# Performance work log

Measured on AMD Instinct MI355X. Metric: run time of the kernel, lower is better.

Reference implementation:

```python
import jax, jax.numpy as jnp
import numpy as np
import math

DIM = 2048
N_HEADS = 32
N_KV_HEADS = 8
HEAD_DIM = DIM // N_HEADS  # 64
N_REP = N_HEADS // N_KV_HEADS  # 4
BSZ, SEQ = 2, 2048


def setup_inputs() -> dict:
    key = jax.random.key(0)
    ks = jax.random.split(key, 8)
    x = jax.random.normal(ks[0], (BSZ, SEQ, DIM), dtype=jnp.float32)
    # rotary tables, [seq, head_dim//2]
    inv_freq = 1.0 / (10000.0 ** (np.arange(0, HEAD_DIM, 2, dtype=np.float32) / HEAD_DIM))
    t = np.arange(SEQ, dtype=np.float32)
    freqs = np.outer(t, inv_freq)
    freqs_cos = jnp.asarray(np.cos(freqs))
    freqs_sin = jnp.asarray(np.sin(freqs))
    s = 0.02
    wq = jax.random.normal(ks[1], (DIM, N_HEADS * HEAD_DIM), dtype=jnp.float32) * s
    wk = jax.random.normal(ks[2], (DIM, N_KV_HEADS * HEAD_DIM), dtype=jnp.float32) * s
    wv = jax.random.normal(ks[3], (DIM, N_KV_HEADS * HEAD_DIM), dtype=jnp.float32) * s
    wo = jax.random.normal(ks[4], (N_HEADS * HEAD_DIM, DIM), dtype=jnp.float32) * s
    return {"x": x, "freqs_cos": freqs_cos, "freqs_sin": freqs_sin,
            "wq": wq, "wk": wk, "wv": wv, "wo": wo}


def _apply_rotary(xq, xk, cos, sin):
    # xq: [b,s,h,d], xk: [b,s,kh,d]; cos/sin: [s, d//2]
    def rot(t):
        tr = t[..., 0::2]  # even -> real
        ti = t[..., 1::2]  # odd  -> imag
        c = cos[None, :, None, :]
        s_ = sin[None, :, None, :]
        or_ = tr * c - ti * s_
        oi_ = tr * s_ + ti * c
        # interleave back: [..., d//2, 2] -> [..., d]
        return jnp.stack([or_, oi_], axis=-1).reshape(t.shape)
    return rot(xq), rot(xk)


def reference(x, freqs_cos, freqs_sin, wq, wk, wv, wo):
    b, s, _ = x.shape
    xq = (x @ wq).reshape(b, s, N_HEADS, HEAD_DIM)
    xk = (x @ wk).reshape(b, s, N_KV_HEADS, HEAD_DIM)
    xv = (x @ wv).reshape(b, s, N_KV_HEADS, HEAD_DIM)
    xq, xk = _apply_rotary(xq, xk, freqs_cos, freqs_sin)
    # repeat_kv: [b,s,kh,d] -> [b,s,kh*n_rep,d]
    xk = jnp.repeat(xk, N_REP, axis=2)
    xv = jnp.repeat(xv, N_REP, axis=2)
    # [b,h,s,d]
    q = xq.transpose(0, 2, 1, 3)
    k = xk.transpose(0, 2, 1, 3)
    v = xv.transpose(0, 2, 1, 3)
    scale = 1.0 / math.sqrt(HEAD_DIM)
    scores = jnp.einsum('bhqd,bhkd->bhqk', q, k) * scale
    causal = jnp.tril(jnp.ones((s, s), dtype=bool))
    scores = jnp.where(causal[None, None], scores, jnp.float32(-jnp.inf))
    probs = jax.nn.softmax(scores, axis=-1)
    out = jnp.einsum('bhqk,bhkd->bhqd', probs, v)  # [b,h,s,d]
    out = out.transpose(0, 2, 1, 3).reshape(b, s, N_HEADS * HEAD_DIM)
    return out @ wo
```

## Files before the change

kernel.cpp:

```cpp
#include <hip/hip_runtime.h>
#include <hip/hip_bf16.h>

typedef __attribute__((ext_vector_type(8))) short short8;
typedef __attribute__((ext_vector_type(4))) float f32x4;

__device__ __forceinline__ unsigned short f2bf(float f) {
  union { float f; unsigned u; } v; v.f = f;
  unsigned r = v.u + 0x7FFFu + ((v.u >> 16) & 1u);
  return (unsigned short)(r >> 16);
}
__device__ __forceinline__ float bf2f(unsigned short h) {
  union { unsigned u; float f; } v; v.u = ((unsigned)h) << 16;
  return v.f;
}
__device__ __forceinline__ unsigned pkbf(float a, float b) {
  __hip_bfloat162 h = __float22bfloat162_rn(float2{a, b});
  union { __hip_bfloat162 h; unsigned u; } cv; cv.h = h;
  return cv.u;
}

__global__ void prep(const float* __restrict__ x, const float* __restrict__ wq,
                     const float* __restrict__ wk, const float* __restrict__ wv,
                     const float* __restrict__ wo, unsigned short* __restrict__ xb,
                     unsigned short* __restrict__ wt, unsigned short* __restrict__ wot) {
  const int z = blockIdx.z, tid = threadIdx.x;
  if (z == 0) {
    int id = blockIdx.y * 64 + blockIdx.x;
#pragma unroll
    for (int rep = 0; rep < 2; ++rep) {
      int i = (rep * 4096 + id) * 256 + tid;
      float4 v = ((const float4*)x)[i];
      ushort4 o;
      o.x = f2bf(v.x); o.y = f2bf(v.y); o.z = f2bf(v.z); o.w = f2bf(v.w);
      ((ushort4*)xb)[i] = o;
    }
    return;
  }
  __shared__ float tile[32][33];
  const float* src;
  unsigned short* dst;
  int N;
  if (z == 1) { src = wq; dst = wt; N = 2048; }
  else if (z == 2) { src = wk; dst = wt + 2048ull * 2048; N = 512; }
  else if (z == 3) { src = wv; dst = wt + 2560ull * 2048; N = 512; }
  else { src = wo; dst = wot; N = 2048; }
  const int K = 2048;
  int n0 = blockIdx.x * 32, k0 = blockIdx.y * 32;
  if (n0 >= N) return;
  int xx = tid & 31, yy = tid >> 5;
#pragma unroll
  for (int j = 0; j < 4; ++j) tile[yy + 8 * j][xx] = src[(size_t)(k0 + yy + 8 * j) * N + n0 + xx];
  __syncthreads();
#pragma unroll
  for (int j = 0; j < 4; ++j) dst[(size_t)(n0 + yy + 8 * j) * K + k0 + xx] = f2bf(tile[xx][yy + 8 * j]);
}

template <int MODE>
__global__ __launch_bounds__(256, 2) void gemm_bt64(const unsigned short* __restrict__ A,
                                                    const unsigned short* __restrict__ Bt,
                                                    void* __restrict__ Cv, int K, int ldc,
                                                    unsigned short* __restrict__ vt) {
  __shared__ alignas(16) unsigned short As[128 * 64];
  __shared__ alignas(16) unsigned short Bs[128 * 64];
  const int t = threadIdx.x;
  const int lane = t & 63, w = t >> 6;
  const int l15 = lane & 15, quad = lane >> 4;
  const int bn0 = blockIdx.x * 128, bm0 = blockIdx.y * 128;
  const int wm = (w >> 1) * 64, wn = (w & 1) * 64;
  const unsigned short* Ab = A + (size_t)bm0 * K;
  const unsigned short* Bb = Bt + (size_t)bn0 * K;
  const int asw = l15 & 7;

  f32x4 acc[4][4];
  const f32x4 zf = {0.f, 0.f, 0.f, 0.f};
#pragma unroll
  for (int i = 0; i < 4; ++i)
#pragma unroll
    for (int j = 0; j < 4; ++j) acc[i][j] = zf;

  for (int k0 = 0; k0 < K; k0 += 64) {
    __syncthreads();
#pragma unroll
    for (int r = 0; r < 4; ++r) {
      int e = r * 256 + t;
      int row = e >> 3, cslot = e & 7;
      int cg = cslot ^ (row & 7);
      const unsigned short* ga = Ab + (size_t)row * K + k0 + cg * 8;
      __builtin_amdgcn_global_load_lds((const __attribute__((address_space(1))) void*)ga,
                                       (__attribute__((address_space(3))) void*)(As + e * 8), 16, 0, 0);
      const unsigned short* gb = Bb + (size_t)row * K + k0 + cg * 8;
      __builtin_amdgcn_global_load_lds((const __attribute__((address_space(1))) void*)gb,
                                       (__attribute__((address_space(3))) void*)(Bs + e * 8), 16, 0, 0);
    }
    __syncthreads();
#pragma unroll
    for (int s = 0; s < 2; ++s) {
      short8 af[4], bf[4];
#pragma unroll
      for (int i = 0; i < 4; ++i)
        af[i] = *reinterpret_cast<const short8*>(As + (wm + i * 16 + l15) * 64 + (((s * 4 + quad) ^ asw) * 8));
#pragma unroll
      for (int j = 0; j < 4; ++j)
        bf[j] = *reinterpret_cast<const short8*>(Bs + (wn + j * 16 + l15) * 64 + (((s * 4 + quad) ^ asw) * 8));
#pragma unroll
      for (int i = 0; i < 4; ++i)
#pragma unroll
        for (int j = 0; j < 4; ++j)
          acc[i][j] = __builtin_amdgcn_mfma_f32_16x16x32_bf16(af[i], bf[j], acc[i][j], 0, 0, 0);
    }
  }

  if (MODE == 1 && bn0 >= 2560) {
    const int b = bm0 >> 11;
#pragma unroll
    for (int i = 0; i < 4; ++i) {
      int srow = (bm0 + wm + i * 16 + quad * 4) & 2047;
#pragma unroll
      for (int j = 0; j < 4; ++j) {
        int vcol = bn0 - 2560 + wn + j * 16 + l15;
        int kvh = vcol >> 6, d = vcol & 63;
        uint2 pk = make_uint2(pkbf(acc[i][j][0], acc[i][j][1]), pkbf(acc[i][j][2], acc[i][j][3]));
        *reinterpret_cast<uint2*>(vt + ((size_t)(b * 8 + kvh) * 64 + d) * 2048 + srow) = pk;
      }
    }
  } else {
#pragma unroll
    for (int i = 0; i < 4; ++i)
#pragma unroll
      for (int j = 0; j < 4; ++j)
#pragma unroll
        for (int r = 0; r < 4; ++r) {
          size_t row = (size_t)(bm0 + wm + i * 16 + quad * 4 + r);
          size_t col = (size_t)(bn0 + wn + j * 16 + l15);
          if (MODE == 1)
            ((unsigned short*)Cv)[row * ldc + col] = f2bf(acc[i][j][r]);
          else
            ((float*)Cv)[row * ldc + col] = acc[i][j][r];
        }
  }
}

__global__ void rope_k(unsigned short* __restrict__ qkv, const float* __restrict__ fcos,
                       const float* __restrict__ fsin) {
  int tid = blockIdx.x * 256 + threadIdx.x;
  int row = tid >> 8, p = tid & 255;
  int col = 2048 + 2 * p;
  int s = row & 2047;
  int fi = p & 31;
  float c = fcos[s * 32 + fi], sn = fsin[s * 32 + fi];
  unsigned int* ptr = (unsigned int*)(qkv + (size_t)row * 2560 + col);
  unsigned int pr = *ptr;
  float xr = bf2f((unsigned short)(pr & 0xFFFFu));
  float xi = bf2f((unsigned short)(pr >> 16));
  float orr = xr * c - xi * sn;
  float oi = xr * sn + xi * c;
  *ptr = ((unsigned)f2bf(oi) << 16) | (unsigned)f2bf(orr);
}

__global__ __launch_bounds__(256, 4) void flash_attn(const unsigned short* __restrict__ qkv,
                                                     const unsigned short* __restrict__ vt,
                                                     const float* __restrict__ fcos,
                                                     const float* __restrict__ fsin,
                                                     unsigned short* __restrict__ out) {
  __shared__ alignas(16) unsigned short Ks[64 * 64];
  __shared__ alignas(16) unsigned short Vs[64 * 64];
  __shared__ alignas(16) unsigned short Ps[128 * 64];
  __shared__ float Ls[128];
  const int t = threadIdx.x, lane = t & 63, w = t >> 6;
  const int l15 = lane & 15, quad = lane >> 4;
  const int h = blockIdx.y, b = blockIdx.z;
  const int qb = ((int)blockIdx.x ^ (15 * (h >> 4))) & 15;
  const int q0 = qb * 128;
  const int kvh = h >> 2;
  const size_t rowB = (size_t)b * 2048;
  const unsigned short* Qg = qkv + (rowB + q0) * 2560 + h * 64;
  const unsigned short* Kg = qkv + rowB * 2560 + 2048 + kvh * 64;
  const unsigned short* Vtg = vt + (size_t)(b * 8 + kvh) * 64 * 2048;
  const float SC = 0.18033688011112042f;

  short8 qf[2][2];
#pragma unroll
  for (int mt = 0; mt < 2; ++mt)
#pragma unroll
    for (int s = 0; s < 2; ++s) {
      int qrow = w * 32 + mt * 16 + l15;
      short8 raw = *reinterpret_cast<const short8*>(Qg + (size_t)qrow * 2560 + s * 32 + quad * 8);
      f32x4 c4 = *reinterpret_cast<const f32x4*>(fcos + (size_t)(q0 + qrow) * 32 + s * 16 + quad * 4);
      f32x4 s4 = *reinterpret_cast<const f32x4*>(fsin + (size_t)(q0 + qrow) * 32 + s * 16 + quad * 4);
      short8 o;
#pragma unroll
      for (int k = 0; k < 4; ++k) {
        float xr = bf2f((unsigned short)raw[2 * k]);
        float xi = bf2f((unsigned short)raw[2 * k + 1]);
        o[2 * k] = (short)f2bf((xr * c4[k] - xi * s4[k]) * SC);
        o[2 * k + 1] = (short)f2bf((xr * s4[k] + xi * c4[k]) * SC);
      }
      qf[mt][s] = o;
    }

  const f32x4 zf = {0.f, 0.f, 0.f, 0.f};
  f32x4 oacc[2][4];
#pragma unroll
  for (int mt = 0; mt < 2; ++mt)
#pragma unroll
    for (int nt = 0; nt < 4; ++nt) oacc[mt][nt] = zf;
  float lsum[2] = {0.f, 0.f};

  const int kb_end = 2 * qb + 2;
  const int srow = t >> 3, sc8 = t & 7;
  const int soff = srow * 64 + ((sc8 ^ (srow & 7)) * 8);
  const int asw = l15 & 7;
  short8 kreg[2], vreg[2];
#pragma unroll
  for (int r = 0; r < 2; ++r) {
    kreg[r] = *reinterpret_cast<const short8*>(Kg + (size_t)(srow + 32 * r) * 2560 + sc8 * 8);
    vreg[r] = *reinterpret_cast<const short8*>(Vtg + (size_t)(srow + 32 * r) * 2048 + sc8 * 8);
  }

  for (int kb = 0; kb < kb_end; ++kb) {
    __syncthreads();
#pragma unroll
    for (int r = 0; r < 2; ++r) {
      *reinterpret_cast<short8*>(Ks + soff + r * 32 * 64) = kreg[r];
      *reinterpret_cast<short8*>(Vs + soff + r * 32 * 64) = vreg[r];
    }
    __syncthreads();
    if (kb + 1 < kb_end) {
#pragma unroll
      for (int r = 0; r < 2; ++r) {
        kreg[r] = *reinterpret_cast<const short8*>(Kg + (size_t)((kb + 1) * 64 + srow + 32 * r) * 2560 + sc8 * 8);
        vreg[r] = *reinterpret_cast<const short8*>(Vtg + (size_t)(srow + 32 * r) * 2048 + (kb + 1) * 64 + sc8 * 8);
      }
    }
    const int qmaxw = q0 + w * 32 + 31;
    if (kb * 64 > qmaxw) continue;
    const bool needMask = (kb * 64 + 63) > (q0 + w * 32);

#pragma unroll
    for (int kvt = 0; kvt < 4; ++kvt) {
      f32x4 st0 = zf, st1 = zf;
#pragma unroll
      for (int s = 0; s < 2; ++s) {
        short8 kf = *reinterpret_cast<const short8*>(Ks + (kvt * 16 + l15) * 64 + ((s * 4 + quad) ^ asw) * 8);
        st0 = __builtin_amdgcn_mfma_f32_16x16x32_bf16(kf, qf[0][s], st0, 0, 0, 0);
        st1 = __builtin_amdgcn_mfma_f32_16x16x32_bf16(kf, qf[1][s], st1, 0, 0, 0);
      }
      const int pcol = ((kvt * 2 + (quad >> 1)) ^ asw) * 8 + (quad & 1) * 4;
      if (needMask) {
        const int kvb = kb * 64 + kvt * 16 + quad * 4;
#pragma unroll
        for (int qt = 0; qt < 2; ++qt) {
          const f32x4 stv = qt ? st1 : st0;
          const int qg = q0 + w * 32 + qt * 16 + l15;
          float p[4];
#pragma unroll
          for (int r = 0; r < 4; ++r) {
            float pv = __builtin_amdgcn_exp2f(stv[r]);
            p[r] = (kvb + r > qg) ? 0.f : pv;
          }
          lsum[qt] += (p[0] + p[1]) + (p[2] + p[3]);
          *reinterpret_cast<uint2*>(Ps + (size_t)(w * 32 + qt * 16 + l15) * 64 + pcol) =
              make_uint2(pkbf(p[0], p[1]), pkbf(p[2], p[3]));
        }
      } else {
#pragma unroll
        for (int qt = 0; qt < 2; ++qt) {
          const f32x4 stv = qt ? st1 : st0;
          float p[4];
#pragma unroll
          for (int r = 0; r < 4; ++r) p[r] = __builtin_amdgcn_exp2f(stv[r]);
          lsum[qt] += (p[0] + p[1]) + (p[2] + p[3]);
          *reinterpret_cast<uint2*>(Ps + (size_t)(w * 32 + qt * 16 + l15) * 64 + pcol) =
              make_uint2(pkbf(p[0], p[1]), pkbf(p[2], p[3]));
        }
      }
    }

#pragma unroll
    for (int s = 0; s < 2; ++s) {
      short8 vf[4];
#pragma unroll
      for (int nt = 0; nt < 4; ++nt)
        vf[nt] = *reinterpret_cast<const short8*>(Vs + (nt * 16 + l15) * 64 + ((s * 4 + quad) ^ asw) * 8);
#pragma unroll
      for (int mt = 0; mt < 2; ++mt) {
        short8 pf = *reinterpret_cast<const short8*>(Ps + (size_t)(w * 32 + mt * 16 + l15) * 64 + ((s * 4 + quad) ^ asw) * 8);
#pragma unroll
        for (int nt = 0; nt < 4; ++nt)
          oacc[mt][nt] = __builtin_amdgcn_mfma_f32_16x16x32_bf16(pf, vf[nt], oacc[mt][nt], 0, 0, 0);
      }
    }
  }

#pragma unroll
  for (int qt = 0; qt < 2; ++qt) {
    lsum[qt] += __shfl_xor(lsum[qt], 16, 64);
    lsum[qt] += __shfl_xor(lsum[qt], 32, 64);
  }
  if (quad == 0) {
    Ls[w * 32 + l15] = lsum[0];
    Ls[w * 32 + 16 + l15] = lsum[1];
  }
  float linv[2][4];
#pragma unroll
  for (int mt = 0; mt < 2; ++mt)
#pragma unroll
    for (int r = 0; r < 4; ++r) linv[mt][r] = 1.f / Ls[w * 32 + mt * 16 + quad * 4 + r];

#pragma unroll
  for (int mt = 0; mt < 2; ++mt)
#pragma unroll
    for (int nt = 0; nt < 4; ++nt)
#pragma unroll
      for (int r = 0; r < 4; ++r) {
        size_t row = rowB + (size_t)(q0 + w * 32 + mt * 16 + quad * 4 + r);
        size_t col = (size_t)h * 64 + nt * 16 + l15;
        out[row * 2048 + col] = f2bf(oacc[mt][nt][r] * linv[mt][r]);
      }
}

extern "C" void kernel_launch(void* const* d_in, const int* in_sizes, int n_in, void* d_out,
                              int out_size, void* d_ws, size_t ws_size, hipStream_t stream) {
  const float* x = (const float*)d_in[0];
  const float* fcos = (const float*)d_in[1];
  const float* fsin = (const float*)d_in[2];
  const float* wq = (const float*)d_in[3];
  const float* wk = (const float*)d_in[4];
  const float* wv = (const float*)d_in[5];
  const float* wo = (const float*)d_in[6];

  char* ws = (char*)d_ws;
  unsigned short* xb = (unsigned short*)ws;
  unsigned short* wt = (unsigned short*)(ws + 16777216ull);
  unsigned short* wot = (unsigned short*)(ws + 29360128ull);
  unsigned short* qkv = (unsigned short*)(ws + 37748736ull);
  unsigned short* attno = (unsigned short*)(ws + 58720256ull);
  unsigned short* vt = (unsigned short*)(ws + 75497472ull);

  prep<<<dim3(64, 64, 5), 256, 0, stream>>>(x, wq, wk, wv, wo, xb, wt, wot);
  gemm_bt64<1><<<dim3(24, 32), 256, 0, stream>>>(xb, wt, qkv, 2048, 2560, vt);
  rope_k<<<4096, 256, 0, stream>>>(qkv, fcos, fsin);
  flash_attn<<<dim3(16, 32, 2), 256, 0, stream>>>(qkv, vt, fcos, fsin, attno);
  gemm_bt64<0><<<dim3(16, 32), 256, 0, stream>>>(attno, wot, d_out, 2048, 2048, nullptr);
}
```

Measured before the change: 271.0 us.

## Fuse K rope into QKV GEMM epilogue and pair causal query tiles in attention

The K-part rotary embedding moves into the QKV GEMM epilogue, using a lane shuffle to fetch the pair element, and the separate rope kernel is dropped. Flash attention now processes two query tiles per block (qb and 15-qb) so every block does the same causal work. K/V tiles are double-buffered in LDS via global_load_lds async copies, and row sums are computed with an MFMA against a ones vector. The cost is higher register and LDS use, which is why launch bounds drop to 2 blocks per SM, and the grid is halved.

```diff
diff --git a/kernel.cpp b/kernel.cpp
--- a/kernel.cpp
+++ b/kernel.cpp
@@ -59,7 +59,9 @@
 __global__ __launch_bounds__(256, 2) void gemm_bt64(const unsigned short* __restrict__ A,
                                                     const unsigned short* __restrict__ Bt,
                                                     void* __restrict__ Cv, int K, int ldc,
-                                                    unsigned short* __restrict__ vt) {
+                                                    unsigned short* __restrict__ vt,
+                                                    const float* __restrict__ fcos,
+                                                    const float* __restrict__ fsin) {
   __shared__ alignas(16) unsigned short As[128 * 64];
   __shared__ alignas(16) unsigned short Bs[128 * 64];
   const int t = threadIdx.x;
@@ -123,6 +125,23 @@
         *reinterpret_cast<uint2*>(vt + ((size_t)(b * 8 + kvh) * 64 + d) * 2048 + srow) = pk;
       }
     }
+  } else if (MODE == 1 && bn0 >= 2048) {
+#pragma unroll
+    for (int i = 0; i < 4; ++i)
+#pragma unroll
+      for (int j = 0; j < 4; ++j)
+#pragma unroll
+        for (int r = 0; r < 4; ++r) {
+          int row = bm0 + wm + i * 16 + quad * 4 + r;
+          int s = row & 2047;
+          int col = bn0 + wn + j * 16 + l15;
+          int fi = ((col - 2048) >> 1) & 31;
+          float val = acc[i][j][r];
+          float par = __shfl_xor(val, 1, 64);
+          float c = fcos[s * 32 + fi], sn = fsin[s * 32 + fi];
+          float o = (lane & 1) ? (par * sn + val * c) : (val * c - par * sn);
+          ((unsigned short*)Cv)[(size_t)row * ldc + col] = f2bf(o);
+        }
   } else {
 #pragma unroll
     for (int i = 0; i < 4; ++i)
@@ -140,137 +159,153 @@
   }
 }
 
-__global__ void rope_k(unsigned short* __restrict__ qkv, const float* __restrict__ fcos,
-                       const float* __restrict__ fsin) {
-  int tid = blockIdx.x * 256 + threadIdx.x;
-  int row = tid >> 8, p = tid & 255;
-  int col = 2048 + 2 * p;
-  int s = row & 2047;
-  int fi = p & 31;
-  float c = fcos[s * 32 + fi], sn = fsin[s * 32 + fi];
-  unsigned int* ptr = (unsigned int*)(qkv + (size_t)row * 2560 + col);
-  unsigned int pr = *ptr;
-  float xr = bf2f((unsigned short)(pr & 0xFFFFu));
-  float xi = bf2f((unsigned short)(pr >> 16));
-  float orr = xr * c - xi * sn;
-  float oi = xr * sn + xi * c;
-  *ptr = ((unsigned)f2bf(oi) << 16) | (unsigned)f2bf(orr);
-}
-
-__global__ __launch_bounds__(256, 4) void flash_attn(const unsigned short* __restrict__ qkv,
+__global__ __launch_bounds__(256, 2) void flash_attn(const unsigned short* __restrict__ qkv,
                                                      const unsigned short* __restrict__ vt,
                                                      const float* __restrict__ fcos,
                                                      const float* __restrict__ fsin,
                                                      unsigned short* __restrict__ out) {
-  __shared__ alignas(16) unsigned short Ks[64 * 64];
-  __shared__ alignas(16) unsigned short Vs[64 * 64];
-  __shared__ alignas(16) unsigned short Ps[128 * 64];
-  __shared__ float Ls[128];
+  __shared__ alignas(16) unsigned short Ks[2][64 * 64];
+  __shared__ alignas(16) unsigned short Vs[2][64 * 64];
+  __shared__ alignas(16) unsigned short Ps[256 * 64];
   const int t = threadIdx.x, lane = t & 63, w = t >> 6;
   const int l15 = lane & 15, quad = lane >> 4;
   const int h = blockIdx.y, b = blockIdx.z;
-  const int qb = ((int)blockIdx.x ^ (15 * (h >> 4))) & 15;
-  const int q0 = qb * 128;
+  const int qb = blockIdx.x;
+  const int qA0 = qb * 128, qB0 = (15 - qb) * 128;
   const int kvh = h >> 2;
   const size_t rowB = (size_t)b * 2048;
-  const unsigned short* Qg = qkv + (rowB + q0) * 2560 + h * 64;
   const unsigned short* Kg = qkv + rowB * 2560 + 2048 + kvh * 64;
   const unsigned short* Vtg = vt + (size_t)(b * 8 + kvh) * 64 * 2048;
   const float SC = 0.18033688011112042f;
 
-  short8 qf[2][2];
-#pragma unroll
-  for (int mt = 0; mt < 2; ++mt)
-#pragma unroll
-    for (int s = 0; s < 2; ++s) {
-      int qrow = w * 32 + mt * 16 + l15;
-      short8 raw = *reinterpret_cast<const short8*>(Qg + (size_t)qrow * 2560 + s * 32 + quad * 8);
-      f32x4 c4 = *reinterpret_cast<const f32x4*>(fcos + (size_t)(q0 + qrow) * 32 + s * 16 + quad * 4);
-      f32x4 s4 = *reinterpret_cast<const f32x4*>(fsin + (size_t)(q0 + qrow) * 32 + s * 16 + quad * 4);
-      short8 o;
-#pragma unroll
-      for (int k = 0; k < 4; ++k) {
-        float xr = bf2f((unsigned short)raw[2 * k]);
-        float xi = bf2f((unsigned short)raw[2 * k + 1]);
-        o[2 * k] = (short)f2bf((xr * c4[k] - xi * s4[k]) * SC);
-        o[2 * k + 1] = (short)f2bf((xr * s4[k] + xi * c4[k]) * SC);
-      }
-      qf[mt][s] = o;
-    }
+  short8 qfA[2][2], qfB[2][2];
+#pragma unroll
+  for (int tl = 0; tl < 2; ++tl) {
+    const int q0 = tl ? qB0 : qA0;
+    const unsigned short* Qg = qkv + (rowB + q0) * 2560 + h * 64;
+#pragma unroll
+    for (int mt = 0; mt < 2; ++mt)
+#pragma unroll
+      for (int s = 0; s < 2; ++s) {
+        int qrow = w * 32 + mt * 16 + l15;
+        short8 raw = *reinterpret_cast<const short8*>(Qg + (size_t)qrow * 2560 + s * 32 + quad * 8);
+        f32x4 c4 = *reinterpret_cast<const f32x4*>(fcos + (size_t)(q0 + qrow) * 32 + s * 16 + quad * 4);
+        f32x4 s4 = *reinterpret_cast<const f32x4*>(fsin + (size_t)(q0 + qrow) * 32 + s * 16 + quad * 4);
+        short8 o;
+#pragma unroll
+        for (int k = 0; k < 4; ++k) {
+          float xr = bf2f((unsigned short)raw[2 * k]);
+          float xi = bf2f((unsigned short)raw[2 * k + 1]);
+          o[2 * k] = (short)f2bf((xr * c4[k] - xi * s4[k]) * SC);
+          o[2 * k + 1] = (short)f2bf((xr * s4[k] + xi * c4[k]) * SC);
+        }
+        if (tl) qfB[mt][s] = o; else qfA[mt][s] = o;
+      }
+  }
 
   const f32x4 zf = {0.f, 0.f, 0.f, 0.f};
-  f32x4 oacc[2][4];
-#pragma unroll
-  for (int mt = 0; mt < 2; ++mt)
-#pragma unroll
-    for (int nt = 0; nt < 4; ++nt) oacc[mt][nt] = zf;
-  float lsum[2] = {0.f, 0.f};
-
-  const int kb_end = 2 * qb + 2;
-  const int srow = t >> 3, sc8 = t & 7;
-  const int soff = srow * 64 + ((sc8 ^ (srow & 7)) * 8);
+  f32x4 oaccA[2][4], oaccB[2][4], laccA[2], laccB[2];
+#pragma unroll
+  for (int mt = 0; mt < 2; ++mt) {
+    laccA[mt] = zf; laccB[mt] = zf;
+#pragma unroll
+    for (int nt = 0; nt < 4; ++nt) { oaccA[mt][nt] = zf; oaccB[mt][nt] = zf; }
+  }
+  short8 onesf;
+#pragma unroll
+  for (int k = 0; k < 8; ++k) onesf[k] = (short)0x3F80;
+
+  const int kbB_end = 32 - 2 * qb;
   const int asw = l15 & 7;
-  short8 kreg[2], vreg[2];
-#pragma unroll
-  for (int r = 0; r < 2; ++r) {
-    kreg[r] = *reinterpret_cast<const short8*>(Kg + (size_t)(srow + 32 * r) * 2560 + sc8 * 8);
-    vreg[r] = *reinterpret_cast<const short8*>(Vtg + (size_t)(srow + 32 * r) * 2048 + sc8 * 8);
-  }
-
-  for (int kb = 0; kb < kb_end; ++kb) {
+  unsigned short* Ks0 = &Ks[0][0];
+  unsigned short* Ks1 = &Ks[1][0];
+  unsigned short* Vs0 = &Vs[0][0];
+  unsigned short* Vs1 = &Vs[1][0];
+
+  auto stage = [&](int buf, int kb) {
+    unsigned short* kd = buf ? Ks1 : Ks0;
+    unsigned short* vd = buf ? Vs1 : Vs0;
+#pragma unroll
+    for (int r = 0; r < 2; ++r) {
+      int e = r * 256 + t;
+      int row = e >> 3, cs = e & 7;
+      int cg = cs ^ (row & 7);
+      const unsigned short* gk = Kg + (size_t)(kb * 64 + row) * 2560 + cg * 8;
+      __builtin_amdgcn_global_load_lds((const __attribute__((address_space(1))) void*)gk,
+                                       (__attribute__((address_space(3))) void*)(kd + e * 8), 16, 0, 0);
+      const unsigned short* gv = Vtg + (size_t)row * 2048 + kb * 64 + cg * 8;
+      __builtin_amdgcn_global_load_lds((const __attribute__((address_space(1))) void*)gv,
+                                       (__attribute__((address_space(3))) void*)(vd + e * 8), 16, 0, 0);
+    }
+  };
+
+  stage(0, 0);
+
+  for (int kb = 0; kb < kbB_end; ++kb) {
+    const int cur = kb & 1;
     __syncthreads();
-#pragma unroll
-    for (int r = 0; r < 2; ++r) {
-      *reinterpret_cast<short8*>(Ks + soff + r * 32 * 64) = kreg[r];
-      *reinterpret_cast<short8*>(Vs + soff + r * 32 * 64) = vreg[r];
-    }
-    __syncthreads();
-    if (kb + 1 < kb_end) {
-#pragma unroll
-      for (int r = 0; r < 2; ++r) {
-        kreg[r] = *reinterpret_cast<const short8*>(Kg + (size_t)((kb + 1) * 64 + srow + 32 * r) * 2560 + sc8 * 8);
-        vreg[r] = *reinterpret_cast<const short8*>(Vtg + (size_t)(srow + 32 * r) * 2048 + (kb + 1) * 64 + sc8 * 8);
-      }
-    }
-    const int qmaxw = q0 + w * 32 + 31;
-    if (kb * 64 > qmaxw) continue;
-    const bool needMask = (kb * 64 + 63) > (q0 + w * 32);
+    if (kb + 1 < kbB_end) stage(cur ^ 1, kb + 1);
+    const unsigned short* Kc = cur ? Ks1 : Ks0;
+    const unsigned short* Vc = cur ? Vs1 : Vs0;
+    const bool actA = kb * 64 <= qA0 + w * 32 + 31;
+    const bool actB = kb * 64 <= qB0 + w * 32 + 31;
+    const bool mA = (kb * 64 + 63) > (qA0 + w * 32);
+    const bool mB = (kb * 64 + 63) > (qB0 + w * 32);
 
 #pragma unroll
     for (int kvt = 0; kvt < 4; ++kvt) {
-      f32x4 st0 = zf, st1 = zf;
+      f32x4 sA0 = zf, sA1 = zf, sB0 = zf, sB1 = zf;
 #pragma unroll
       for (int s = 0; s < 2; ++s) {
-        short8 kf = *reinterpret_cast<const short8*>(Ks + (kvt * 16 + l15) * 64 + ((s * 4 + quad) ^ asw) * 8);
-        st0 = __builtin_amdgcn_mfma_f32_16x16x32_bf16(kf, qf[0][s], st0, 0, 0, 0);
-        st1 = __builtin_amdgcn_mfma_f32_16x16x32_bf16(kf, qf[1][s], st1, 0, 0, 0);
+        short8 kf = *reinterpret_cast<const short8*>(Kc + (kvt * 16 + l15) * 64 + ((s * 4 + quad) ^ asw) * 8);
+        if (actA) {
+          sA0 = __builtin_amdgcn_mfma_f32_16x16x32_bf16(kf, qfA[0][s], sA0, 0, 0, 0);
+          sA1 = __builtin_amdgcn_mfma_f32_16x16x32_bf16(kf, qfA[1][s], sA1, 0, 0, 0);
+        }
+        if (actB) {
+          sB0 = __builtin_amdgcn_mfma_f32_16x16x32_bf16(kf, qfB[0][s], sB0, 0, 0, 0);
+          sB1 = __builtin_amdgcn_mfma_f32_16x16x32_bf16(kf, qfB[1][s], sB1, 0, 0, 0);
+        }
       }
       const int pcol = ((kvt * 2 + (quad >> 1)) ^ asw) * 8 + (quad & 1) * 4;
-      if (needMask) {
-        const int kvb = kb * 64 + kvt * 16 + quad * 4;
+      const int kvb = kb * 64 + kvt * 16 + quad * 4;
+      if (actA) {
 #pragma unroll
         for (int qt = 0; qt < 2; ++qt) {
-          const f32x4 stv = qt ? st1 : st0;
-          const int qg = q0 + w * 32 + qt * 16 + l15;
+          const f32x4 stv = qt ? sA1 : sA0;
           float p[4];
-#pragma unroll
-          for (int r = 0; r < 4; ++r) {
-            float pv = __builtin_amdgcn_exp2f(stv[r]);
-            p[r] = (kvb + r > qg) ? 0.f : pv;
+          if (mA) {
+            const int qg = qA0 + w * 32 + qt * 16 + l15;
+#pragma unroll
+            for (int r = 0; r < 4; ++r) {
+              float pv = __builtin_amdgcn_exp2f(stv[r]);
+              p[r] = (kvb + r > qg) ? 0.f : pv;
+            }
+          } else {
+#pragma unroll
+            for (int r = 0; r < 4; ++r) p[r] = __builtin_amdgcn_exp2f(stv[r]);
           }
-          lsum[qt] += (p[0] + p[1]) + (p[2] + p[3]);
           *reinterpret_cast<uint2*>(Ps + (size_t)(w * 32 + qt * 16 + l15) * 64 + pcol) =
               make_uint2(pkbf(p[0], p[1]), pkbf(p[2], p[3]));
         }
-      } else {
+      }
+      if (actB) {
 #pragma unroll
         for (int qt = 0; qt < 2; ++qt) {
-          const f32x4 stv = qt ? st1 : st0;
+          const f32x4 stv = qt ? sB1 : sB0;
           float p[4];
-#pragma unroll
-          for (int r = 0; r < 4; ++r) p[r] = __builtin_amdgcn_exp2f(stv[r]);
-          lsum[qt] += (p[0] + p[1]) + (p[2] + p[3]);
-          *reinterpret_cast<uint2*>(Ps + (size_t)(w * 32 + qt * 16 + l15) * 64 + pcol) =
+          if (mB) {
+            const int qg = qB0 + w * 32 + qt * 16 + l15;
+#pragma unroll
+            for (int r = 0; r < 4; ++r) {
+              float pv = __builtin_amdgcn_exp2f(stv[r]);
+              p[r] = (kvb + r > qg) ? 0.f : pv;
+            }
+          } else {
+#pragma unroll
+            for (int r = 0; r < 4; ++r) p[r] = __builtin_amdgcn_exp2f(stv[r]);
+          }
+          *reinterpret_cast<uint2*>(Ps + (size_t)(128 + w * 32 + qt * 16 + l15) * 64 + pcol) =
               make_uint2(pkbf(p[0], p[1]), pkbf(p[2], p[3]));
         }
       }
@@ -281,42 +316,49 @@
       short8 vf[4];
 #pragma unroll
       for (int nt = 0; nt < 4; ++nt)
-        vf[nt] = *reinterpret_cast<const short8*>(Vs + (nt * 16 + l15) * 64 + ((s * 4 + quad) ^ asw) * 8);
-#pragma unroll
-      for (int mt = 0; mt < 2; ++mt) {
-        short8 pf = *reinterpret_cast<const short8*>(Ps + (size_t)(w * 32 + mt * 16 + l15) * 64 + ((s * 4 + quad) ^ asw) * 8);
-#pragma unroll
-        for (int nt = 0; nt < 4; ++nt)
-          oacc[mt][nt] = __builtin_amdgcn_mfma_f32_16x16x32_bf16(pf, vf[nt], oacc[mt][nt], 0, 0, 0);
-      }
-    }
-  }
-
-#pragma unroll
-  for (int qt = 0; qt < 2; ++qt) {
-    lsum[qt] += __shfl_xor(lsum[qt], 16, 64);
-    lsum[qt] += __shfl_xor(lsum[qt], 32, 64);
-  }
-  if (quad == 0) {
-    Ls[w * 32 + l15] = lsum[0];
-    Ls[w * 32 + 16 + l15] = lsum[1];
-  }
-  float linv[2][4];
-#pragma unroll
-  for (int mt = 0; mt < 2; ++mt)
-#pragma unroll
-    for (int r = 0; r < 4; ++r) linv[mt][r] = 1.f / Ls[w * 32 + mt * 16 + quad * 4 + r];
-
-#pragma unroll
-  for (int mt = 0; mt < 2; ++mt)
-#pragma unroll
-    for (int nt = 0; nt < 4; ++nt)
+        vf[nt] = *reinterpret_cast<const short8*>(Vc + (nt * 16 + l15) * 64 + ((s * 4 + quad) ^ asw) * 8);
+      if (actA) {
+#pragma unroll
+        for (int mt = 0; mt < 2; ++mt) {
+          short8 pf = *reinterpret_cast<const short8*>(Ps + (size_t)(w * 32 + mt * 16 + l15) * 64 + ((s * 4 + quad) ^ asw) * 8);
+#pragma unroll
+          for (int nt = 0; nt < 4; ++nt)
+            oaccA[mt][nt] = __builtin_amdgcn_mfma_f32_16x16x32_bf16(pf, vf[nt], oaccA[mt][nt], 0, 0, 0);
+          laccA[mt] = __builtin_amdgcn_mfma_f32_16x16x32_bf16(pf, onesf, laccA[mt], 0, 0, 0);
+        }
+      }
+      if (actB) {
+#pragma unroll
+        for (int mt = 0; mt < 2; ++mt) {
+          short8 pf = *reinterpret_cast<const short8*>(Ps + (size_t)(128 + w * 32 + mt * 16 + l15) * 64 + ((s * 4 + quad) ^ asw) * 8);
+#pragma unroll
+          for (int nt = 0; nt < 4; ++nt)
+            oaccB[mt][nt] = __builtin_amdgcn_mfma_f32_16x16x32_bf16(pf, vf[nt], oaccB[mt][nt], 0, 0, 0);
+          laccB[mt] = __builtin_amdgcn_mfma_f32_16x16x32_bf16(pf, onesf, laccB[mt], 0, 0, 0);
+        }
+      }
+    }
+  }
+
+#pragma unroll
+  for (int tl = 0; tl < 2; ++tl) {
+    const int q0 = tl ? qB0 : qA0;
+#pragma unroll
+    for (int mt = 0; mt < 2; ++mt) {
+      const f32x4 lv = tl ? laccB[mt] : laccA[mt];
 #pragma unroll
       for (int r = 0; r < 4; ++r) {
+        const float linv = 1.f / lv[r];
         size_t row = rowB + (size_t)(q0 + w * 32 + mt * 16 + quad * 4 + r);
-        size_t col = (size_t)h * 64 + nt * 16 + l15;
-        out[row * 2048 + col] = f2bf(oacc[mt][nt][r] * linv[mt][r]);
-      }
+#pragma unroll
+        for (int nt = 0; nt < 4; ++nt) {
+          const f32x4 ov = tl ? oaccB[mt][nt] : oaccA[mt][nt];
+          size_t col = (size_t)h * 64 + nt * 16 + l15;
+          out[row * 2048 + col] = f2bf(ov[r] * linv);
+        }
+      }
+    }
+  }
 }
 
 extern "C" void kernel_launch(void* const* d_in, const int* in_sizes, int n_in, void* d_out,
@@ -338,8 +380,7 @@
   unsigned short* vt = (unsigned short*)(ws + 75497472ull);
 
   prep<<<dim3(64, 64, 5), 256, 0, stream>>>(x, wq, wk, wv, wo, xb, wt, wot);
-  gemm_bt64<1><<<dim3(24, 32), 256, 0, stream>>>(xb, wt, qkv, 2048, 2560, vt);
-  rope_k<<<4096, 256, 0, stream>>>(qkv, fcos, fsin);
-  flash_attn<<<dim3(16, 32, 2), 256, 0, stream>>>(qkv, vt, fcos, fsin, attno);
-  gemm_bt64<0><<<dim3(16, 32), 256, 0, stream>>>(attno, wot, d_out, 2048, 2048, nullptr);
-}
+  gemm_bt64<1><<<dim3(24, 32), 256, 0, stream>>>(xb, wt, qkv, 2048, 2560, vt, fcos, fsin);
+  flash_attn<<<dim3(8, 32, 2), 256, 0, stream>>>(qkv, vt, fcos, fsin, attno);
+  gemm_bt64<0><<<dim3(16, 32), 256, 0, stream>>>(attno, wot, d_out, 2048, 2048, nullptr, nullptr, nullptr);
+}
```

After: 296.2 us. 1.09x slower.

## Fuse K rotary into QKV GEMM epilogue, compute row sums via MFMA, add setprio

Applied to the files above, without the earlier changes.

The separate rope_k kernel is dropped. RoPE for the K columns is now applied inside the QKV GEMM epilogue, using a lane shuffle to fetch each element's interleaved partner before the bf16 store. In flash attention, the softmax denominator is now accumulated by an extra MFMA of P against a ones vector. This replaces the per-lane scalar sums, cross-lane shuffles and the LDS reduction. s_setprio hints are also wrapped around the MFMA blocks to favor matrix issue, at the cost of one extra MFMA per P tile.

```diff
diff --git a/kernel.cpp b/kernel.cpp
--- a/kernel.cpp
+++ b/kernel.cpp
@@ -59,7 +59,9 @@
 __global__ __launch_bounds__(256, 2) void gemm_bt64(const unsigned short* __restrict__ A,
                                                     const unsigned short* __restrict__ Bt,
                                                     void* __restrict__ Cv, int K, int ldc,
-                                                    unsigned short* __restrict__ vt) {
+                                                    unsigned short* __restrict__ vt,
+                                                    const float* __restrict__ fcos,
+                                                    const float* __restrict__ fsin) {
   __shared__ alignas(16) unsigned short As[128 * 64];
   __shared__ alignas(16) unsigned short Bs[128 * 64];
   const int t = threadIdx.x;
@@ -102,11 +104,13 @@
 #pragma unroll
       for (int j = 0; j < 4; ++j)
         bf[j] = *reinterpret_cast<const short8*>(Bs + (wn + j * 16 + l15) * 64 + (((s * 4 + quad) ^ asw) * 8));
+      __builtin_amdgcn_s_setprio(1);
 #pragma unroll
       for (int i = 0; i < 4; ++i)
 #pragma unroll
         for (int j = 0; j < 4; ++j)
           acc[i][j] = __builtin_amdgcn_mfma_f32_16x16x32_bf16(af[i], bf[j], acc[i][j], 0, 0, 0);
+      __builtin_amdgcn_s_setprio(0);
     }
   }
 
@@ -123,6 +127,23 @@
         *reinterpret_cast<uint2*>(vt + ((size_t)(b * 8 + kvh) * 64 + d) * 2048 + srow) = pk;
       }
     }
+  } else if (MODE == 1 && bn0 >= 2048) {
+#pragma unroll
+    for (int i = 0; i < 4; ++i)
+#pragma unroll
+      for (int j = 0; j < 4; ++j)
+#pragma unroll
+        for (int r = 0; r < 4; ++r) {
+          int row = bm0 + wm + i * 16 + quad * 4 + r;
+          int s = row & 2047;
+          int col = bn0 + wn + j * 16 + l15;
+          int fi = ((col - 2048) >> 1) & 31;
+          float val = acc[i][j][r];
+          float par = __shfl_xor(val, 1, 64);
+          float c = fcos[s * 32 + fi], sn = fsin[s * 32 + fi];
+          float o = (lane & 1) ? (par * sn + val * c) : (val * c - par * sn);
+          ((unsigned short*)Cv)[(size_t)row * ldc + col] = f2bf(o);
+        }
   } else {
 #pragma unroll
     for (int i = 0; i < 4; ++i)
@@ -140,23 +161,6 @@
   }
 }
 
-__global__ void rope_k(unsigned short* __restrict__ qkv, const float* __restrict__ fcos,
-                       const float* __restrict__ fsin) {
-  int tid = blockIdx.x * 256 + threadIdx.x;
-  int row = tid >> 8, p = tid & 255;
-  int col = 2048 + 2 * p;
-  int s = row & 2047;
-  int fi = p & 31;
-  float c = fcos[s * 32 + fi], sn = fsin[s * 32 + fi];
-  unsigned int* ptr = (unsigned int*)(qkv + (size_t)row * 2560 + col);
-  unsigned int pr = *ptr;
-  float xr = bf2f((unsigned short)(pr & 0xFFFFu));
-  float xi = bf2f((unsigned short)(pr >> 16));
-  float orr = xr * c - xi * sn;
-  float oi = xr * sn + xi * c;
-  *ptr = ((unsigned)f2bf(oi) << 16) | (unsigned)f2bf(orr);
-}
-
 __global__ __launch_bounds__(256, 4) void flash_attn(const unsigned short* __restrict__ qkv,
                                                      const unsigned short* __restrict__ vt,
                                                      const float* __restrict__ fcos,
@@ -165,7 +169,6 @@
   __shared__ alignas(16) unsigned short Ks[64 * 64];
   __shared__ alignas(16) unsigned short Vs[64 * 64];
   __shared__ alignas(16) unsigned short Ps[128 * 64];
-  __shared__ float Ls[128];
   const int t = threadIdx.x, lane = t & 63, w = t >> 6;
   const int l15 = lane & 15, quad = lane >> 4;
   const int h = blockIdx.y, b = blockIdx.z;
@@ -199,12 +202,16 @@
     }
 
   const f32x4 zf = {0.f, 0.f, 0.f, 0.f};
-  f32x4 oacc[2][4];
-#pragma unroll
-  for (int mt = 0; mt < 2; ++mt)
+  f32x4 oacc[2][4], lacc[2];
+#pragma unroll
+  for (int mt = 0; mt < 2; ++mt) {
+    lacc[mt] = zf;
 #pragma unroll
     for (int nt = 0; nt < 4; ++nt) oacc[mt][nt] = zf;
-  float lsum[2] = {0.f, 0.f};
+  }
+  short8 onesf;
+#pragma unroll
+  for (int k = 0; k < 8; ++k) onesf[k] = (short)0x3F80;
 
   const int kb_end = 2 * qb + 2;
   const int srow = t >> 3, sc8 = t & 7;
@@ -242,8 +249,10 @@
 #pragma unroll
       for (int s = 0; s < 2; ++s) {
         short8 kf = *reinterpret_cast<const short8*>(Ks + (kvt * 16 + l15) * 64 + ((s * 4 + quad) ^ asw) * 8);
+        __builtin_amdgcn_s_setprio(1);
         st0 = __builtin_amdgcn_mfma_f32_16x16x32_bf16(kf, qf[0][s], st0, 0, 0, 0);
         st1 = __builtin_amdgcn_mfma_f32_16x16x32_bf16(kf, qf[1][s], st1, 0, 0, 0);
+        __builtin_amdgcn_s_setprio(0);
       }
       const int pcol = ((kvt * 2 + (quad >> 1)) ^ asw) * 8 + (quad & 1) * 4;
       if (needMask) {
@@ -258,7 +267,6 @@
             float pv = __builtin_amdgcn_exp2f(stv[r]);
             p[r] = (kvb + r > qg) ? 0.f : pv;
           }
-          lsum[qt] += (p[0] + p[1]) + (p[2] + p[3]);
           *reinterpret_cast<uint2*>(Ps + (size_t)(w * 32 + qt * 16 + l15) * 64 + pcol) =
               make_uint2(pkbf(p[0], p[1]), pkbf(p[2], p[3]));
         }
@@ -269,7 +277,6 @@
           float p[4];
 #pragma unroll
           for (int r = 0; r < 4; ++r) p[r] = __builtin_amdgcn_exp2f(stv[r]);
-          lsum[qt] += (p[0] + p[1]) + (p[2] + p[3]);
           *reinterpret_cast<uint2*>(Ps + (size_t)(w * 32 + qt * 16 + l15) * 64 + pcol) =
               make_uint2(pkbf(p[0], p[1]), pkbf(p[2], p[3]));
         }
@@ -285,27 +292,21 @@
 #pragma unroll
       for (int mt = 0; mt < 2; ++mt) {
         short8 pf = *reinterpret_cast<const short8*>(Ps + (size_t)(w * 32 + mt * 16 + l15) * 64 + ((s * 4 + quad) ^ asw) * 8);
+        __builtin_amdgcn_s_setprio(1);
 #pragma unroll
         for (int nt = 0; nt < 4; ++nt)
           oacc[mt][nt] = __builtin_amdgcn_mfma_f32_16x16x32_bf16(pf, vf[nt], oacc[mt][nt], 0, 0, 0);
-      }
-    }
-  }
-
-#pragma unroll
-  for (int qt = 0; qt < 2; ++qt) {
-    lsum[qt] += __shfl_xor(lsum[qt], 16, 64);
-    lsum[qt] += __shfl_xor(lsum[qt], 32, 64);
-  }
-  if (quad == 0) {
-    Ls[w * 32 + l15] = lsum[0];
-    Ls[w * 32 + 16 + l15] = lsum[1];
-  }
+        lacc[mt] = __builtin_amdgcn_mfma_f32_16x16x32_bf16(pf, onesf, lacc[mt], 0, 0, 0);
+        __builtin_amdgcn_s_setprio(0);
+      }
+    }
+  }
+
   float linv[2][4];
 #pragma unroll
   for (int mt = 0; mt < 2; ++mt)
 #pragma unroll
-    for (int r = 0; r < 4; ++r) linv[mt][r] = 1.f / Ls[w * 32 + mt * 16 + quad * 4 + r];
+    for (int r = 0; r < 4; ++r) linv[mt][r] = 1.f / lacc[mt][r];
 
 #pragma unroll
   for (int mt = 0; mt < 2; ++mt)
@@ -338,8 +339,7 @@
   unsigned short* vt = (unsigned short*)(ws + 75497472ull);
 
   prep<<<dim3(64, 64, 5), 256, 0, stream>>>(x, wq, wk, wv, wo, xb, wt, wot);
-  gemm_bt64<1><<<dim3(24, 32), 256, 0, stream>>>(xb, wt, qkv, 2048, 2560, vt);
-  rope_k<<<4096, 256, 0, stream>>>(qkv, fcos, fsin);
+  gemm_bt64<1><<<dim3(24, 32), 256, 0, stream>>>(xb, wt, qkv, 2048, 2560, vt, fcos, fsin);
   flash_attn<<<dim3(16, 32, 2), 256, 0, stream>>>(qkv, vt, fcos, fsin, attno);
-  gemm_bt64<0><<<dim3(16, 32), 256, 0, stream>>>(attno, wot, d_out, 2048, 2048, nullptr);
-}
+  gemm_bt64<0><<<dim3(16, 32), 256, 0, stream>>>(attno, wot, d_out, 2048, 2048, nullptr, nullptr, nullptr);
+}
```

Result: no change. 266.3 us (-1.8%).
